# Performance work log

Measured on AMD Instinct MI355X. Metric: run time of the kernel, lower is better.

The kernel has to match this reference:

```python
import jax, jax.numpy as jnp
import numpy as np
import math

H = 512        # hidden_size (channels)
N = 64         # state_size
MAX_LEN = 4096 # kernel length L
BATCH = 8
SEQ = 4096     # seq len of input (== MAX_LEN here)


def _nplr(n):
    # HiPPO-LegS NPLR decomposition (done once at init, numpy float64 for eig stability)
    i = np.arange(n, dtype=np.float64)
    j = np.sqrt(2 * i + 1)
    A = -(np.tril(j[None, :] * j[:, None]) - np.diag(i))
    Bv = j.astype(np.complex128)
    p = j / np.sqrt(2.0)
    w, V = np.linalg.eig(A + p[None, :] * p[:, None])  # normal part; conj-pair eigvals adjacent
    w = w[::2].copy()          # [N/2]
    V = V[:, ::2].copy()       # [N, N/2]
    Bc = V.conj().T @ Bv       # [N/2]
    pc = V.conj().T @ p.astype(np.complex128)
    V_full = np.concatenate([V, V.conj()], axis=-1)      # [N, N]
    VtAV = V_full.conj().T @ A.astype(np.complex128) @ V_full  # [N, N]
    return w, pc, V, Bc, VtAV


def _ri(c):
    # complex -> trailing real/imag pair, float32 (mirrors torch.view_as_real)
    return np.stack([c.real, c.imag], axis=-1).astype(np.float32)


def setup_inputs() -> dict:
    rng = np.random.default_rng(0)
    w, p, V, Bc, Amat = _nplr(N)
    Brep = np.tile(Bc[None, :], (H, 1))                      # [H, N/2]
    C = rng.standard_normal((H, N)).astype(np.complex128)
    C = C @ V.conj()                                         # einsum('hn,nm->hm') -> [H, N/2]
    log_dt = math.log(1e-3) + (math.log(1e-1) - math.log(1e-3)) * rng.random(H)
    dt = np.exp(log_dt)[:, None, None]
    I = np.eye(N, dtype=np.complex128)[None]
    dA = np.linalg.inv(I - dt * Amat / 2) @ (I + dt * Amat / 2)   # [H, N, N]
    dA_power = I - np.linalg.matrix_power(dA, MAX_LEN)
    C2 = np.concatenate([C, C.conj()], axis=-1)              # [H, N]
    C2 = np.einsum('hmn,hm->hn', dA_power.conj(), C2)[:, : N // 2]
    p_rep = np.tile(p[None, None, :], (H, 1, 1))             # [H, 1, N/2]
    Bfull = np.concatenate([Brep[:, None, :], p_rep], axis=1)  # [H, 2, N/2]
    Cfull = np.concatenate([C2[:, None, :], p_rep], axis=1)    # [H, 2, N/2] (q == p)

    key = jax.random.key(0)
    kx, kd = jax.random.split(key)
    return {
        "x": jax.random.normal(kx, (BATCH, SEQ, H), dtype=jnp.float32),
        "log_dt": jnp.asarray(log_dt, dtype=jnp.float32),   # [H]
        "w_ri": jnp.asarray(_ri(w)),                        # [N/2, 2]
        "B_ri": jnp.asarray(_ri(Bfull)),                    # [H, 2, N/2, 2]
        "C_ri": jnp.asarray(_ri(Cfull)),                    # [H, 2, N/2, 2]
        "D": jax.random.normal(kd, (H,), dtype=jnp.float32),
    }


def _s4_kernel(log_dt, w_ri, B_ri, C_ri):
    L = MAX_LEN
    w = w_ri[..., 0] + 1j * w_ri[..., 1]   # [n] with n = N/2
    B = B_ri[..., 0] + 1j * B_ri[..., 1]   # [H, 2, n]
    C = C_ri[..., 0] + 1j * C_ri[..., 1]   # [H, 2, n]
    dt = jnp.exp(log_dt)                   # [H]
    freq = jnp.exp(-2j * jnp.pi / L * jnp.arange(L // 2 + 1))  # [F], F = L/2+1
    z = 2 * (1 - freq) / (1 + freq)        # bilinear-transformed frequencies

    v = C[:, :, None, :].conj() * B[:, None, :, :]   # [H, 2, 2, n]
    wd = w[None, :] * dt[:, None]                    # [H, n]
    # cauchy_mult: r = sum_n v/(z-w) + conj(v)/(z-conj(w)), as batched matmuls over n
    K1 = 1.0 / (z[None, None, :] - wd[:, :, None])          # [H, n, F]
    K2 = 1.0 / (z[None, None, :] - wd.conj()[:, :, None])   # [H, n, F]
    r = jnp.einsum('habn,hnf->habf', v, K1) + jnp.einsum('habn,hnf->habf', v.conj(), K2)
    r = r * dt[:, None, None, None]
    # Woodbury correction for the rank-1 (p, q) augmentation
    k_f = r[:, 0, 0, :] - r[:, 0, 1, :] * r[:, 1, 0, :] / (1 + r[:, 1, 1, :])  # [H, F]
    k_f = k_f * 2 / (1 + freq)
    return jnp.fft.irfft(k_f)   # [H, L]


def reference(x, log_dt, w_ri, B_ri, C_ri, D):
    k = _s4_kernel(log_dt, w_ri, B_ri, C_ri)     # [H, L]
    xt = jnp.transpose(x, (0, 2, 1))             # [B, H, Lx]
    L2 = 2 * MAX_LEN                              # conv pads to 2*kernel_len
    k_f = jnp.fft.rfft(k, n=L2)                  # [H, L2/2+1]
    x_f = jnp.fft.rfft(xt, n=L2)                 # [B, H, L2/2+1]
    y = jnp.fft.irfft(k_f[None] * x_f, n=L2)[..., : xt.shape[-1]]
    y = y + xt * D[None, :, None]                # skip connection
    return jnp.transpose(y, (0, 2, 1))           # [B, Lx, H]
```

## Files before the change

kernel.cpp:

```cpp
#include <hip/hip_runtime.h>
#include <math.h>

#define TPB 256
#define CTPB 512
#define KTPB 512

__device__ __forceinline__ float2 cmul(float2 a, float2 b) {
    return make_float2(a.x * b.x - a.y * b.y, a.x * b.y + a.y * b.x);
}
__device__ __forceinline__ float2 cdivf(float2 a, float2 b) {
    float inv = 1.0f / (b.x * b.x + b.y * b.y);
    return make_float2((a.x * b.x + a.y * b.y) * inv, (a.y * b.x - a.x * b.y) * inv);
}
__device__ __forceinline__ float2 cadd(float2 a, float2 b) { return make_float2(a.x + b.x, a.y + b.y); }
__device__ __forceinline__ float2 csub(float2 a, float2 b) { return make_float2(a.x - b.x, a.y - b.y); }
__device__ __forceinline__ float2 mul_i(float2 a, float d) {
    return make_float2(-d * a.y, d * a.x);
}
__device__ __forceinline__ int brev11(int x) { return (int)(__brev((unsigned)x) >> 21); }
__device__ __forceinline__ int rev8(int x) {
    return ((x & 7) << 9) | (((x >> 3) & 7) << 6) | (((x >> 6) & 7) << 3) | ((x >> 9) & 7);
}
__device__ __forceinline__ int swz(int i) { return i ^ ((i >> 4) & 15) ^ ((i >> 8) & 15); }

__device__ __forceinline__ void dft8(const float2* x, float2* y, float d) {
    const float r = 0.70710678118f;
    float2 s0 = cadd(x[0], x[4]), t0 = csub(x[0], x[4]);
    float2 s1 = cadd(x[1], x[5]), t1 = csub(x[1], x[5]);
    float2 s2 = cadd(x[2], x[6]), t2 = csub(x[2], x[6]);
    float2 s3 = cadd(x[3], x[7]), t3 = csub(x[3], x[7]);
    t1 = cmul(t1, make_float2(r, d * r));
    t2 = mul_i(t2, d);
    t3 = cmul(t3, make_float2(-r, d * r));
    float2 u0 = cadd(s0, s2), v0 = csub(s0, s2);
    float2 u1 = cadd(s1, s3), v1 = mul_i(csub(s1, s3), d);
    y[0] = cadd(u0, u1); y[4] = csub(u0, u1);
    y[2] = cadd(v0, v1); y[6] = csub(v0, v1);
    float2 p0 = cadd(t0, t2), q0 = csub(t0, t2);
    float2 p1 = cadd(t1, t3), q1 = mul_i(csub(t1, t3), d);
    y[1] = cadd(p0, p1); y[5] = csub(p0, p1);
    y[3] = cadd(q0, q1); y[7] = csub(q0, q1);
}

__device__ __forceinline__ void dft8z(float2 x0, float2 x1, float2 x2, float2 x3,
                                      float2* y, float d) {
    const float r = 0.70710678118f;
    float2 u0 = cadd(x0, x2), v0 = csub(x0, x2);
    float2 u1 = cadd(x1, x3), v1 = mul_i(csub(x1, x3), d);
    float2 t1 = cmul(x1, make_float2(r, d * r));
    float2 t2 = mul_i(x2, d);
    float2 t3 = cmul(x3, make_float2(-r, d * r));
    float2 p0 = cadd(x0, t2), q0 = csub(x0, t2);
    float2 p1 = cadd(t1, t3), q1 = mul_i(csub(t1, t3), d);
    y[0] = cadd(u0, u1); y[4] = csub(u0, u1);
    y[2] = cadd(v0, v1); y[6] = csub(v0, v1);
    y[1] = cadd(p0, p1); y[5] = csub(p0, p1);
    y[3] = cadd(q0, q1); y[7] = csub(q0, q1);
}

__device__ __forceinline__ void dft8_lo(const float2* x, float2* y, float d) {
    const float r = 0.70710678118f;
    float2 s0 = cadd(x[0], x[4]), t0 = csub(x[0], x[4]);
    float2 s1 = cadd(x[1], x[5]), t1 = csub(x[1], x[5]);
    float2 s2 = cadd(x[2], x[6]), t2 = csub(x[2], x[6]);
    float2 s3 = cadd(x[3], x[7]), t3 = csub(x[3], x[7]);
    t1 = cmul(t1, make_float2(r, d * r));
    t2 = mul_i(t2, d);
    t3 = cmul(t3, make_float2(-r, d * r));
    float2 u0 = cadd(s0, s2), v0 = csub(s0, s2);
    float2 u1 = cadd(s1, s3), v1 = mul_i(csub(s1, s3), d);
    y[0] = cadd(u0, u1);
    y[2] = cadd(v0, v1);
    float2 p0 = cadd(t0, t2), q0 = csub(t0, t2);
    float2 p1 = cadd(t1, t3), q1 = mul_i(csub(t1, t3), d);
    y[1] = cadd(p0, p1);
    y[3] = cadd(q0, q1);
}

template <int HB, int DIR>
__device__ __forceinline__ void dif_stage(float2* s, int tid) {
    __syncthreads();
    const int h = 1 << HB;
    int j = tid & (h - 1);
    int base = ((tid >> HB) << (HB + 3)) + j;
    int s0 = swz(base);
    float2 x[8];
#pragma unroll
    for (int k = 0; k < 8; ++k) x[k] = s[s0 ^ swz(k << HB)];
    float2 y[8];
    dft8(x, y, (float)DIR);
    if constexpr (HB != 0) {
        float ang = (float)DIR * 6.283185307179586f / (float)(h << 3) * (float)j;
        float c, sn;
        __sincosf(ang, &sn, &c);
        float2 w = make_float2(c, sn), wm = w;
        s[s0] = y[0];
#pragma unroll
        for (int m = 1; m < 8; ++m) {
            s[s0 ^ swz(m << HB)] = cmul(wm, y[m]);
            wm = cmul(wm, w);
        }
    } else {
#pragma unroll
        for (int m = 0; m < 8; ++m) s[s0 ^ swz(m << HB)] = y[m];
    }
}

template <int HB, int DIR>
__device__ __forceinline__ void dit_stage(float2* s, int tid) {
    __syncthreads();
    const int h = 1 << HB;
    int j = tid & (h - 1);
    int base = ((tid >> HB) << (HB + 3)) + j;
    int s0 = swz(base);
    float2 x[8];
    if constexpr (HB != 0) {
        float ang = (float)DIR * 6.283185307179586f / (float)(h << 3) * (float)j;
        float c, sn;
        __sincosf(ang, &sn, &c);
        float2 w = make_float2(c, sn);
        x[0] = s[s0];
        float2 wm = w;
#pragma unroll
        for (int k = 1; k < 8; ++k) {
            x[k] = cmul(wm, s[s0 ^ swz(k << HB)]);
            wm = cmul(wm, w);
        }
    } else {
#pragma unroll
        for (int k = 0; k < 8; ++k) x[k] = s[s0 ^ swz(k << HB)];
    }
    float2 y[8];
    dft8(x, y, (float)DIR);
#pragma unroll
    for (int m = 0; m < 8; ++m) s[s0 ^ swz(m << HB)] = y[m];
}

template <int LOGN, int NT>
__device__ void fft8_dif(float2* s, int tid, float dir) {
    const int N = 1 << LOGN;
#pragma unroll
    for (int hb = LOGN - 3; hb >= 0; hb -= 3) {
        const int h = 1 << hb;
        const float astep = dir * 6.283185307179586f / (float)(h << 3);
        __syncthreads();
#pragma unroll
        for (int it = 0; it < (N >> 3) / NT; ++it) {
            const int b = tid + it * NT;
            int j = b & (h - 1);
            int base = ((b >> hb) << (hb + 3)) + j;
            int s0 = swz(base);
            float2 x[8];
#pragma unroll
            for (int k = 0; k < 8; ++k) x[k] = s[s0 ^ swz(k << hb)];
            float2 y[8];
            dft8(x, y, dir);
            if (hb != 0) {
                float ang = astep * (float)j;
                float c, sn;
                __sincosf(ang, &sn, &c);
                float2 w = make_float2(c, sn), wm = w;
                s[s0] = y[0];
#pragma unroll
                for (int m = 1; m < 8; ++m) {
                    s[s0 ^ swz(m << hb)] = cmul(wm, y[m]);
                    wm = cmul(wm, w);
                }
            } else {
#pragma unroll
                for (int m = 0; m < 8; ++m) s[s0 ^ swz(m << hb)] = y[m];
            }
        }
    }
    __syncthreads();
}

template <int LOGN, int NT>
__device__ void fft_dif2(float2* s, int tid, float dir) {
    const int N = 1 << LOGN;
    for (int st = LOGN - 1; st >= 0; --st) {
        __syncthreads();
        int half = 1 << st;
        for (int b = tid; b < (N >> 1); b += NT) {
            int j  = b & (half - 1);
            int i0 = ((b >> st) << (st + 1)) + j;
            int i1 = i0 + half;
            float2 u = s[i0], v = s[i1];
            float2 d = make_float2(u.x - v.x, u.y - v.y);
            s[i0] = make_float2(u.x + v.x, u.y + v.y);
            if (half > 1) {
                float ang = dir * 3.14159265358979f * (float)j / (float)half;
                float c, sn;
                __sincosf(ang, &sn, &c);
                s[i1] = cmul(make_float2(c, sn), d);
            } else {
                s[i1] = d;
            }
        }
    }
    __syncthreads();
}

__global__ __launch_bounds__(TPB) void kf_kernel(
    const float* __restrict__ log_dt, const float* __restrict__ w_ri,
    const float* __restrict__ Bri, const float* __restrict__ Cri,
    float2* __restrict__ kf) {
    __shared__ float2 wds[32];
    __shared__ float aab[4][32], rab[4][32];
    __shared__ float qn[32], pn[32];
    const int h   = blockIdx.x;
    const int tid = threadIdx.x;
    const float dt = expf(log_dt[h]);
    if (tid < 32) {
        float wr = w_ri[2 * tid] * dt, wi = w_ri[2 * tid + 1] * dt;
        wds[tid] = make_float2(wr, wi);
        qn[tid]  = wr * wr + wi * wi;
        pn[tid]  = -2.0f * wr;
    }
    __syncthreads();
    if (tid < 128) {
        int a = tid >> 6, b = (tid >> 5) & 1, n = tid & 31;
        const float* Cp = Cri + (((h * 2 + a) * 32) + n) * 2;
        const float* Bp = Bri + (((h * 2 + b) * 32) + n) * 2;
        float Cr = Cp[0], Ci = Cp[1], Br = Bp[0], Bi = Bp[1];
        float2 v = make_float2(Cr * Br + Ci * Bi, Cr * Bi - Ci * Br);
        float2 wd = wds[n];
        aab[a * 2 + b][n] = -2.0f * (v.x * wd.x + v.y * wd.y);
        rab[a * 2 + b][n] = 2.0f * v.x;
    }
    __syncthreads();
    const int by   = blockIdx.y;
    const int fend = (by == 3) ? 2049 : (by + 1) * 512;
    for (int f = by * 512 + tid; f < fend; f += TPB) {
        float th = (6.283185307179586f / 4096.0f) * (float)f;
        float cf = cosf(th), sf = sinf(th);
        float2 den = make_float2(1.0f + cf, -sf);
        float zt  = 2.0f * tanf(0.5f * th);
        float zt2 = zt * zt;
        float2 r00 = make_float2(0.f, 0.f), r01 = r00, r10 = r00, r11 = r00;
        for (int n = 0; n < 32; ++n) {
            float c   = qn[n] - zt2;
            float d   = pn[n] * zt;
            float inv = 1.0f / (c * c + d * d);
            float cc = c * inv, dd = d * inv;
            float a0 = aab[0][n], b0 = rab[0][n] * zt;
            r00.x += a0 * cc + b0 * dd; r00.y += b0 * cc - a0 * dd;
            float a1 = aab[1][n], b1 = rab[1][n] * zt;
            r01.x += a1 * cc + b1 * dd; r01.y += b1 * cc - a1 * dd;
            float a2 = aab[2][n], b2 = rab[2][n] * zt;
            r10.x += a2 * cc + b2 * dd; r10.y += b2 * cc - a2 * dd;
            float a3 = aab[3][n], b3 = rab[3][n] * zt;
            r11.x += a3 * cc + b3 * dd; r11.y += b3 * cc - a3 * dd;
        }
        r00.x *= dt; r00.y *= dt; r01.x *= dt; r01.y *= dt;
        r10.x *= dt; r10.y *= dt; r11.x *= dt; r11.y *= dt;
        float2 q  = cdivf(cmul(r01, r10), make_float2(1.0f + r11.x, r11.y));
        float2 k0 = make_float2(r00.x - q.x, r00.y - q.y);
        float2 kv = cmul(k0, cdivf(make_float2(2.0f, 0.0f), den));
        kf[h * 2049 + f] = kv;
    }
}

__global__ __launch_bounds__(KTPB) void kprep_kernel(const float2* __restrict__ kf,
                                                     float2* __restrict__ Kt) {
    __shared__ float2 s[4096];
    const int hh = blockIdx.x, tid = threadIdx.x;
    const float2* X = kf + hh * 2049;
    for (int m = tid; m < 2048; m += KTPB) {
        float2 Xm = X[m];
        float2 Xc = X[2048 - m];
        if (m == 0) { Xm.y = 0.0f; Xc.y = 0.0f; }
        float2 A  = make_float2(Xm.x + Xc.x, Xm.y - Xc.y);
        float2 Bv = make_float2(Xm.x - Xc.x, Xm.y + Xc.y);
        float ang = (3.14159265358979f / 2048.0f) * (float)m;
        float c, sn;
        __sincosf(ang, &sn, &c);
        float2 O = cmul(make_float2(c, sn), Bv);
        s[m] = make_float2(0.5f * (A.x - O.y), 0.5f * (A.y + O.x));
    }
    fft_dif2<11, KTPB>(s, tid, +1.0f);
    float2 reg[4];
    const float sc = 1.0f / 2048.0f;
#pragma unroll
    for (int i = 0; i < 4; ++i) {
        int t = tid + KTPB * i;
        float2 v = s[brev11(t)];
        reg[i] = make_float2(v.x * sc, v.y * sc);
    }
    __syncthreads();
#pragma unroll
    for (int i = 0; i < 4; ++i) {
        int t = tid + KTPB * i;
        s[swz(t)]        = reg[i];
        s[swz(t + 2048)] = make_float2(0.f, 0.f);
    }
    fft8_dif<12, KTPB>(s, tid, -1.0f);
    float2* K = Kt + (size_t)hh * 4097;
    for (int p = tid; p < 4096; p += KTPB) {
        int j  = rev8(p);
        int jc = (4096 - j) & 4095;
        int pc = rev8(jc);
        float2 Yj = s[swz(p)], Yc = s[swz(pc)];
        float2 A  = make_float2(Yj.x + Yc.x, Yj.y - Yc.y);
        float2 Bv = make_float2(Yj.x - Yc.x, Yj.y + Yc.y);
        float ang = -(3.14159265358979f / 4096.0f) * (float)j;
        float c, sn;
        __sincosf(ang, &sn, &c);
        float2 t2 = cmul(make_float2(c, sn), make_float2(Bv.y, -Bv.x));
        K[p] = make_float2(0.5f * (A.x + t2.x), 0.5f * (A.y + t2.y));
        if (p == 0) K[4096] = make_float2(Yj.x - Yj.y, 0.0f);
    }
}

__global__ __launch_bounds__(TPB) void transpose_in(const float* __restrict__ x,
                                                    float* __restrict__ xt) {
    __shared__ float tile[64][65];
    const int b = blockIdx.z, t0 = blockIdx.y * 64, h0 = blockIdx.x * 64;
    const int tid = threadIdx.x;
    const float4* xv = (const float4*)(x + ((size_t)b * 4096 + t0) * 512 + h0);
#pragma unroll
    for (int i = 0; i < 4; ++i) {
        int idx = tid + TPB * i;
        int tl = idx >> 4, hq = idx & 15;
        float4 v = xv[(size_t)tl * 128 + hq];
        tile[tl][hq * 4 + 0] = v.x; tile[tl][hq * 4 + 1] = v.y;
        tile[tl][hq * 4 + 2] = v.z; tile[tl][hq * 4 + 3] = v.w;
    }
    __syncthreads();
    float* xo = xt + ((size_t)(b * 512 + h0)) * 4096 + t0;
#pragma unroll
    for (int i = 0; i < 4; ++i) {
        int idx = tid + TPB * i;
        int hl = idx >> 4, tq = idx & 15;
        float4 v = make_float4(tile[tq * 4 + 0][hl], tile[tq * 4 + 1][hl],
                               tile[tq * 4 + 2][hl], tile[tq * 4 + 3][hl]);
        ((float4*)(xo + (size_t)hl * 4096))[tq] = v;
    }
}

__global__ __launch_bounds__(CTPB) void conv_kernel(const float* xt,
                                                    const float2* __restrict__ Kt,
                                                    const float* __restrict__ Dv,
                                                    float* yt) {
    __shared__ float2 s[4096];
    const int row = blockIdx.x, tid = threadIdx.x;
    const int hch = row & 511;
    const int stid = swz(tid);
    const float2* xr = (const float2*)(xt + (size_t)row * 4096);

    {
        float2 x0 = xr[tid], x1 = xr[tid + 512], x2 = xr[tid + 1024], x3 = xr[tid + 1536];
        float2 y[8];
        dft8z(x0, x1, x2, x3, y, -1.0f);
        float ang = -(6.283185307179586f / 4096.0f) * (float)tid;
        float c, sn;
        __sincosf(ang, &sn, &c);
        float2 w = make_float2(c, sn), wm = w;
        s[stid] = y[0];
#pragma unroll
        for (int m = 1; m < 8; ++m) {
            s[stid ^ swz(m << 9)] = cmul(wm, y[m]);
            wm = cmul(wm, w);
        }
    }
    dif_stage<6, -1>(s, tid);
    dif_stage<3, -1>(s, tid);
    dif_stage<0, -1>(s, tid);
    __syncthreads();
    const float2* K = Kt + (size_t)hch * 4097;
#pragma unroll
    for (int i = 0; i < 8; ++i) {
        int p  = tid + CTPB * i;
        int sp = stid ^ swz(CTPB * i);
        if (p == 0) {
            float2 Y0 = s[sp];
            float X0 = Y0.x + Y0.y;
            float Xn = Y0.x - Y0.y;
            float Z0 = X0 * K[0].x;
            float Zn = Xn * K[4096].x;
            s[sp] = make_float2(0.5f * (Z0 + Zn), 0.5f * (Z0 - Zn));
            continue;
        }
        int j  = rev8(p);
        int jc = 4096 - j;
        int pc = rev8(jc & 4095);
        if (pc < p) continue;
        float2 Yj = s[sp], Yc = s[swz(pc)];
        float2 A  = make_float2(Yj.x + Yc.x, Yj.y - Yc.y);
        float2 Bv = make_float2(Yj.x - Yc.x, Yj.y + Yc.y);
        float ang = -(3.14159265358979f / 4096.0f) * (float)j;
        float c, sn;
        __sincosf(ang, &sn, &c);
        float2 W = make_float2(c, sn);
        float2 t2 = cmul(W, make_float2(Bv.y, -Bv.x));
        float2 Xj = make_float2(0.5f * (A.x + t2.x), 0.5f * (A.y + t2.y));
        float2 t2c = cmul(make_float2(-W.x, W.y), make_float2(Bv.y, Bv.x));
        float2 Xc2 = make_float2(0.5f * (A.x + t2c.x), 0.5f * (-A.y + t2c.y));
        float2 Zj = cmul(Xj, K[p]);
        float2 Zc = cmul(Xc2, K[pc]);
        float2 A2 = make_float2(Zj.x + Zc.x, Zj.y - Zc.y);
        float2 B2 = make_float2(Zj.x - Zc.x, Zj.y + Zc.y);
        float2 O2 = cmul(make_float2(W.x, -W.y), B2);
        s[sp] = make_float2(0.5f * (A2.x - O2.y), 0.5f * (A2.y + O2.x));
        if (pc != p) {
            float2 O2c = cmul(make_float2(-W.x, -W.y), make_float2(-B2.x, B2.y));
            s[swz(pc)] = make_float2(0.5f * (A2.x - O2c.y), 0.5f * (-A2.y + O2c.x));
        }
    }
    dit_stage<0, 1>(s, tid);
    dit_stage<3, 1>(s, tid);
    dit_stage<6, 1>(s, tid);
    __syncthreads();
    {
        float ang = (6.283185307179586f / 4096.0f) * (float)tid;
        float c, sn;
        __sincosf(ang, &sn, &c);
        float2 w = make_float2(c, sn);
        float2 x[8];
        x[0] = s[stid];
        float2 wm = w;
#pragma unroll
        for (int k = 1; k < 8; ++k) {
            x[k] = cmul(wm, s[stid ^ swz(k << 9)]);
            wm = cmul(wm, w);
        }
        float2 y[4];
        dft8_lo(x, y, 1.0f);
        const float D = Dv[hch];
        float2* yo = (float2*)(yt + (size_t)row * 4096);
        const float sc = 1.0f / 4096.0f;
#pragma unroll
        for (int m = 0; m < 4; ++m) {
            int t2 = tid + (m << 9);
            float2 xin = xr[t2];
            yo[t2] = make_float2(y[m].x * sc + D * xin.x, y[m].y * sc + D * xin.y);
        }
    }
}

__global__ __launch_bounds__(TPB) void transpose_out(const float* __restrict__ yt,
                                                     float* __restrict__ out) {
    __shared__ float tile[64][65];
    const int b = blockIdx.z, t0 = blockIdx.y * 64, h0 = blockIdx.x * 64;
    const int tid = threadIdx.x;
    const float* yp = yt + ((size_t)(b * 512 + h0)) * 4096 + t0;
#pragma unroll
    for (int i = 0; i < 4; ++i) {
        int idx = tid + TPB * i;
        int hl = idx >> 4, tq = idx & 15;
        float4 v = ((const float4*)(yp + (size_t)hl * 4096))[tq];
        tile[tq * 4 + 0][hl] = v.x; tile[tq * 4 + 1][hl] = v.y;
        tile[tq * 4 + 2][hl] = v.z; tile[tq * 4 + 3][hl] = v.w;
    }
    __syncthreads();
    float4* ov = (float4*)(out + ((size_t)b * 4096 + t0) * 512 + h0);
#pragma unroll
    for (int i = 0; i < 4; ++i) {
        int idx = tid + TPB * i;
        int tl = idx >> 4, hq = idx & 15;
        float4 v = make_float4(tile[tl][4 * hq + 0], tile[tl][4 * hq + 1],
                               tile[tl][4 * hq + 2], tile[tl][4 * hq + 3]);
        ov[(size_t)tl * 128 + hq] = v;
    }
}

extern "C" void kernel_launch(void* const* d_in, const int* in_sizes, int n_in,
                              void* d_out, int out_size, void* d_ws, size_t ws_size,
                              hipStream_t stream) {
    (void)in_sizes; (void)n_in; (void)out_size; (void)ws_size;
    const float* x      = (const float*)d_in[0];
    const float* log_dt = (const float*)d_in[1];
    const float* w_ri   = (const float*)d_in[2];
    const float* Bri    = (const float*)d_in[3];
    const float* Cri    = (const float*)d_in[4];
    const float* Dv     = (const float*)d_in[5];
    float* out = (float*)d_out;

    char* ws = (char*)d_ws;
    float*  xt = (float*)(ws);
    float2* kf = (float2*)(ws + 67108864);
    float2* Kt = (float2*)(ws + 75501568);

    kf_kernel<<<dim3(512, 4), TPB, 0, stream>>>(log_dt, w_ri, Bri, Cri, kf);
    kprep_kernel<<<512, KTPB, 0, stream>>>(kf, Kt);
    transpose_in<<<dim3(8, 64, 8), TPB, 0, stream>>>(x, xt);
    conv_kernel<<<4096, CTPB, 0, stream>>>(xt, Kt, Dv, xt);
    transpose_out<<<dim3(8, 64, 8), TPB, 0, stream>>>(xt, out);
}
```

Before: 282.6 us.

## Fold real-FFT twiddles into precomputed fp16 filter coefficients for pointwise multiply

The kernel-prep stage now precomputes, per frequency bin, two complex coefficients (alpha, beta) that absorb the real-FFT unpacking twiddles and the filter response. The convolution's pointwise step then becomes Y_j*alpha + conj(Y_c)*beta, with no sincos or extra complex multiplies per bin, and the p==0 special case is removed. The coefficients are stored as packed half2 pairs so each bin still costs one 8-byte load. This trades fp16 precision in the filter for fewer ALU operations in the conv kernel, which may cost accuracy.

Result: slower. 300.2 us (+6.2%).

```diff
diff --git a/kernel.cpp b/kernel.cpp
--- a/kernel.cpp
+++ b/kernel.cpp
@@ -1,4 +1,5 @@
 #include <hip/hip_runtime.h>
+#include <hip/hip_fp16.h>
 #include <math.h>
 
 #define TPB 256
@@ -7,6 +8,9 @@
 
 __device__ __forceinline__ float2 cmul(float2 a, float2 b) {
     return make_float2(a.x * b.x - a.y * b.y, a.x * b.y + a.y * b.x);
+}
+__device__ __forceinline__ float2 cmulcj(float2 a, float2 b) {
+    return make_float2(a.x * b.x + a.y * b.y, a.y * b.x - a.x * b.y);
 }
 __device__ __forceinline__ float2 cdivf(float2 a, float2 b) {
     float inv = 1.0f / (b.x * b.x + b.y * b.y);
@@ -262,7 +266,7 @@
 }
 
 __global__ __launch_bounds__(KTPB) void kprep_kernel(const float2* __restrict__ kf,
-                                                     float2* __restrict__ Kt) {
+                                                     float2* __restrict__ Ct) {
     __shared__ float2 s[4096];
     const int hh = blockIdx.x, tid = threadIdx.x;
     const float2* X = kf + hh * 2049;
@@ -295,7 +299,7 @@
         s[swz(t + 2048)] = make_float2(0.f, 0.f);
     }
     fft8_dif<12, KTPB>(s, tid, -1.0f);
-    float2* K = Kt + (size_t)hh * 4097;
+    float2* C = Ct + (size_t)hh * 4096;
     for (int p = tid; p < 4096; p += KTPB) {
         int j  = rev8(p);
         int jc = (4096 - j) & 4095;
@@ -307,8 +311,14 @@
         float c, sn;
         __sincosf(ang, &sn, &c);
         float2 t2 = cmul(make_float2(c, sn), make_float2(Bv.y, -Bv.x));
-        K[p] = make_float2(0.5f * (A.x + t2.x), 0.5f * (A.y + t2.y));
-        if (p == 0) K[4096] = make_float2(Yj.x - Yj.y, 0.0f);
+        float2 al = make_float2(0.5f * (A.x + sn * t2.x), 0.5f * (A.y + sn * t2.y));
+        float2 be = make_float2(-0.5f * c * t2.y, 0.5f * c * t2.x);
+        __half2 ha = __floats2half2_rn(al.x, al.y);
+        __half2 hb = __floats2half2_rn(be.x, be.y);
+        float2 raw;
+        *(__half2*)&raw.x = ha;
+        *(__half2*)&raw.y = hb;
+        C[p] = raw;
     }
 }
 
@@ -339,7 +349,7 @@
 }
 
 __global__ __launch_bounds__(CTPB) void conv_kernel(const float* xt,
-                                                    const float2* __restrict__ Kt,
+                                                    const float2* __restrict__ Ct,
                                                     const float* __restrict__ Dv,
                                                     float* yt) {
     __shared__ float2 s[4096];
@@ -367,44 +377,26 @@
     dif_stage<3, -1>(s, tid);
     dif_stage<0, -1>(s, tid);
     __syncthreads();
-    const float2* K = Kt + (size_t)hch * 4097;
+    const float2* C = Ct + (size_t)hch * 4096;
+    const int J0 = rev8(tid);
 #pragma unroll
     for (int i = 0; i < 8; ++i) {
         int p  = tid + CTPB * i;
         int sp = stid ^ swz(CTPB * i);
-        if (p == 0) {
-            float2 Y0 = s[sp];
-            float X0 = Y0.x + Y0.y;
-            float Xn = Y0.x - Y0.y;
-            float Z0 = X0 * K[0].x;
-            float Zn = Xn * K[4096].x;
-            s[sp] = make_float2(0.5f * (Z0 + Zn), 0.5f * (Z0 - Zn));
-            continue;
-        }
-        int j  = rev8(p);
-        int jc = 4096 - j;
-        int pc = rev8(jc & 4095);
+        int j  = J0 + i;
+        int jc = (4096 - j) & 4095;
+        int pc = rev8(jc);
         if (pc < p) continue;
         float2 Yj = s[sp], Yc = s[swz(pc)];
-        float2 A  = make_float2(Yj.x + Yc.x, Yj.y - Yc.y);
-        float2 Bv = make_float2(Yj.x - Yc.x, Yj.y + Yc.y);
-        float ang = -(3.14159265358979f / 4096.0f) * (float)j;
-        float c, sn;
-        __sincosf(ang, &sn, &c);
-        float2 W = make_float2(c, sn);
-        float2 t2 = cmul(W, make_float2(Bv.y, -Bv.x));
-        float2 Xj = make_float2(0.5f * (A.x + t2.x), 0.5f * (A.y + t2.y));
-        float2 t2c = cmul(make_float2(-W.x, W.y), make_float2(Bv.y, Bv.x));
-        float2 Xc2 = make_float2(0.5f * (A.x + t2c.x), 0.5f * (-A.y + t2c.y));
-        float2 Zj = cmul(Xj, K[p]);
-        float2 Zc = cmul(Xc2, K[pc]);
-        float2 A2 = make_float2(Zj.x + Zc.x, Zj.y - Zc.y);
-        float2 B2 = make_float2(Zj.x - Zc.x, Zj.y + Zc.y);
-        float2 O2 = cmul(make_float2(W.x, -W.y), B2);
-        s[sp] = make_float2(0.5f * (A2.x - O2.y), 0.5f * (A2.y + O2.x));
+        float2 raw = C[p];
+        float2 al = __half22float2(*(const __half2*)&raw.x);
+        float2 be = __half22float2(*(const __half2*)&raw.y);
+        s[sp] = cadd(cmul(al, Yj), cmulcj(be, Yc));
         if (pc != p) {
-            float2 O2c = cmul(make_float2(-W.x, -W.y), make_float2(-B2.x, B2.y));
-            s[swz(pc)] = make_float2(0.5f * (A2.x - O2c.y), 0.5f * (-A2.y + O2c.x));
+            float2 rawc = C[pc];
+            float2 alc = __half22float2(*(const __half2*)&rawc.x);
+            float2 bec = __half22float2(*(const __half2*)&rawc.y);
+            s[swz(pc)] = cadd(cmul(alc, Yc), cmulcj(bec, Yj));
         }
     }
     dit_stage<0, 1>(s, tid);
@@ -479,11 +471,11 @@
     char* ws = (char*)d_ws;
     float*  xt = (float*)(ws);
     float2* kf = (float2*)(ws + 67108864);
-    float2* Kt = (float2*)(ws + 75501568);
+    float2* Ct = (float2*)(ws + 75501568);
 
     kf_kernel<<<dim3(512, 4), TPB, 0, stream>>>(log_dt, w_ri, Bri, Cri, kf);
-    kprep_kernel<<<512, KTPB, 0, stream>>>(kf, Kt);
+    kprep_kernel<<<512, KTPB, 0, stream>>>(kf, Ct);
     transpose_in<<<dim3(8, 64, 8), TPB, 0, stream>>>(x, xt);
-    conv_kernel<<<4096, CTPB, 0, stream>>>(xt, Kt, Dv, xt);
+    conv_kernel<<<4096, CTPB, 0, stream>>>(xt, Ct, Dv, xt);
     transpose_out<<<dim3(8, 64, 8), TPB, 0, stream>>>(xt, out);
 }
```
